# Optimization experiments

Measured on AMD Instinct MI355X. Metric: run time of the kernel, lower is better.

Reference implementation:

```python
import jax, jax.numpy as jnp
import numpy as np

B, N, D, R, W, H, I = 256, 2048, 128, 4, 1, 1024, 1024
CI = I + R * D                       # controller input size (1536)
IF = 2 * D * W + 2 * W + 1 + 4 * R + D * R   # interface size (787)
OPI = H + R * D                      # output_proj input (1536)


def _norm(v):
    # F.normalize(dim=-1): x / max(||x||, eps)
    return v / jnp.maximum(jnp.linalg.norm(v, axis=-1, keepdims=True), 1e-12)


def setup_inputs() -> dict:
    key = jax.random.key(0)
    ks = jax.random.split(key, 16)
    u = lambda k, shape, fan: jax.random.uniform(k, shape, jnp.float32, -1.0 / np.sqrt(fan), 1.0 / np.sqrt(fan))
    return {
        "x": jax.random.normal(ks[0], (B, I), jnp.float32),
        "memory": jax.random.normal(ks[1], (N, D), jnp.float32) * np.sqrt(2.0 / (N + D)),  # xavier-ish
        "usage": jax.random.uniform(ks[2], (N,), jnp.float32),          # usage in [0,1)
        "link": jax.random.normal(ks[3], (N, N), jnp.float32) * 0.01,   # non-trivial link state
        "W_ih": u(ks[4], (4 * H, CI), H),
        "W_hh": u(ks[5], (4 * H, H), H),
        "b_ih": u(ks[6], (4 * H,), H),
        "b_hh": u(ks[7], (4 * H,), H),
        "W_if": u(ks[8], (IF, H), H),
        "b_if": u(ks[9], (IF,), H),
        "W_out": u(ks[10], (H, OPI), OPI),
        "b_out": u(ks[11], (H,), OPI),
    }


def reference(x, memory, usage, link, W_ih, W_hh, b_ih, b_hh, W_if, b_if, W_out, b_out):
    # initial uniform read weights (prev state at first step)
    prev_rw = jnp.full((B, R, N), 1.0 / N, x.dtype)
    read_flat = (prev_rw @ memory).reshape(B, -1)                 # (B, R*D)
    cin = jnp.concatenate([x, read_flat], axis=-1)                # (B, CI)

    # single LSTM step, h0 = c0 = 0, torch gate order i,f,g,o
    g = cin @ W_ih.T + b_ih + b_hh
    gi, gf, gg, go = jnp.split(g, 4, axis=-1)
    c = jax.nn.sigmoid(gi) * jnp.tanh(gg)
    h = jax.nn.sigmoid(go) * jnp.tanh(c)                          # (B, H) controller out

    itf = h @ W_if.T + b_if                                       # (B, IF)
    o = 0
    write_vals = itf[:, o:o + D * W].reshape(B, W, D); o += D * W
    erase = jax.nn.sigmoid(itf[:, o:o + D * W]).reshape(B, W, D); o += D * W
    write_gates = jax.nn.sigmoid(itf[:, o:o + W]); o += W         # (B, W)
    alloc_gate = jax.nn.sigmoid(itf[:, o:o + 1]); o += 1          # (B, 1)
    o += W                                                        # free gates (parsed, unused)
    read_modes = jax.nn.softmax(itf[:, o:o + 3 * R].reshape(B, R, 3), -1); o += 3 * R
    read_str = jax.nn.softplus(itf[:, o:o + R]); o += R           # (B, R)
    read_keys = itf[:, o:o + D * R].reshape(B, R, D)

    # content addressing for the write (strength = 1)
    mem_n = _norm(memory)
    cw = jax.nn.softmax(_norm(write_vals.mean(1)) @ mem_n.T, -1)  # (B, N)

    # allocation weighting: sorted-usage cumprod (per source semantics)
    idx = jnp.argsort(usage)
    su = usage[idx]
    cp = jnp.cumprod(1.0 - su)
    alloc_s = jnp.concatenate([su[:1], su[1:] * cp[:-1]])
    alloc = jnp.zeros_like(usage).at[idx].set(alloc_s)[None, :] * alloc_gate  # (B, N)

    write_w = write_gates[:, :, None] * (0.5 * cw + 0.5 * alloc)[:, None, :]  # (B, W, N)

    # temporal link update: batch-mean of diag-masked outer product, decay 0.9
    lu = jnp.einsum('bwn,bwm->nm', write_w, write_w) / B
    lu = lu * (1.0 - jnp.eye(N, dtype=lu.dtype))
    link_new = link * 0.9 + lu * 0.1

    # memory write (erase then add, batch-mean)
    ev = erase * write_gates[:, :, None]
    av = write_vals * write_gates[:, :, None]
    erase_mat = jnp.einsum('bwn,bwd->nd', write_w, ev) / B
    add_mat = jnp.einsum('bwn,bwd->nd', write_w, av) / B
    mem_new = memory * (1.0 - erase_mat) + add_mat

    # read addressing on updated memory and updated link (all R heads vectorized)
    sim = jnp.einsum('brd,nd->brn', _norm(read_keys), _norm(mem_new))
    content_r = jax.nn.softmax(sim * read_str[:, :, None], -1)    # (B, R, N)
    backward_w = jnp.einsum('brn,nm->brm', prev_rw, link_new)     # mode 1: prev @ L
    forward_w = jnp.einsum('brn,mn->brm', prev_rw, link_new)      # mode 2: prev @ L^T
    new_rw = (read_modes[..., 0:1] * content_r
              + read_modes[..., 1:2] * backward_w
              + read_modes[..., 2:3] * forward_w)                 # (B, R, N)

    read_out = (new_rw @ mem_new).reshape(B, -1)                  # (B, R*D)
    out = jnp.concatenate([h, read_out], axis=-1) @ W_out.T + b_out
    return out
```

## Files before the change

kernel.cpp:

```cpp
#include <hip/hip_runtime.h>
#include <cmath>

#define DEVI __device__ __forceinline__

DEVI float sigm(float x){ return 1.f/(1.f+expf(-x)); }

typedef __attribute__((ext_vector_type(8))) _Float16 half8;
typedef __attribute__((ext_vector_type(4))) _Float16 half4;
typedef __attribute__((ext_vector_type(4))) float float4v;


__global__ void k_zero(float* __restrict__ p, int n){
  int i = blockIdx.x*256 + threadIdx.x;
  if (i < n) p[i] = 0.f;
}

__global__ __launch_bounds__(256) void k_stage1(
    const float* __restrict__ mem, float* __restrict__ cm, _Float16* __restrict__ mem_h,
    const float* __restrict__ usage, float* __restrict__ alloc,
    const float* __restrict__ link, float* __restrict__ rsl, float* __restrict__ csl)
{
  __shared__ float smem[4][132];
  const int blk = blockIdx.x, t = threadIdx.x;
  const int wv = t >> 6, lane = t & 63;

  if (blk < 32){
    int n0 = blk*64;
    float c0 = 0.f, c1 = 0.f;
    for (int r = wv; r < 64; r += 4){
      const float* a = mem + (size_t)(n0+r)*128;
      float x0 = a[lane], x1 = a[lane+64];
      float ss = x0*x0 + x1*x1;
      #pragma unroll
      for (int o = 1; o < 64; o <<= 1) ss += __shfl_xor(ss, o);
      float invn = 1.f / fmaxf(sqrtf(ss), 1e-12f);
      mem_h[(size_t)(n0+r)*128 + lane]      = (_Float16)(x0*invn);
      mem_h[(size_t)(n0+r)*128 + 64 + lane] = (_Float16)(x1*invn);
      c0 += x0; c1 += x1;
    }
    smem[wv][lane] = c0; smem[wv][64+lane] = c1;
    __syncthreads();
    if (t < 128) atomicAdd(&cm[t], smem[0][t]+smem[1][t]+smem[2][t]+smem[3][t]);
  } else if (blk < 160){
    int r0 = (blk - 32)*16;
    int c0 = t*8;
    float colacc[8];
    #pragma unroll
    for (int j = 0; j < 8; j++) colacc[j] = 0.f;
    for (int rg = 0; rg < 16; rg += 4){
      float4v v0[4], v1[4];
      #pragma unroll
      for (int u = 0; u < 4; u++){
        const float* lp = link + (size_t)(r0+rg+u)*2048 + c0;
        v0[u] = *(const float4v*)lp;
        v1[u] = *(const float4v*)(lp+4);
      }
      #pragma unroll
      for (int u = 0; u < 4; u++){
        float s = 0.f;
        #pragma unroll
        for (int j = 0; j < 4; j++){
          colacc[j]   += v0[u][j]; colacc[4+j] += v1[u][j];
          s += v0[u][j] + v1[u][j];
        }
        #pragma unroll
        for (int o = 32; o > 0; o >>= 1) s += __shfl_xor(s, o);
        if (lane == 0) smem[wv][rg+u] = s;
      }
    }
    __syncthreads();
    if (t < 16) rsl[r0+t] = smem[0][t]+smem[1][t]+smem[2][t]+smem[3][t];
    #pragma unroll
    for (int j = 0; j < 8; j++) atomicAdd(&csl[c0+j], colacc[j]);
  } else {
    int n = (blk - 160)*4 + wv;
    float un = usage[n];
    float prod = 1.f;
    #pragma unroll
    for (int i = 0; i < 32; i++){
      int m = lane + i*64;
      float um = usage[m];
      bool before = (um < un) || (um == un && m < n);
      prod *= before ? (1.f - um) : 1.f;
    }
    #pragma unroll
    for (int o = 32; o > 0; o >>= 1) prod *= __shfl_xor(prod, o);
    if (lane == 0) alloc[n] = un * prod;
  }
}

__global__ void k_cin(const float* __restrict__ x, const float* __restrict__ cm, _Float16* __restrict__ cin){
  int idx = blockIdx.x*256 + threadIdx.x;
  int b = idx / 1536, k = idx - b*1536;
  float v = (k < 1024) ? x[b*1024 + k] : cm[(k-1024) & 127] * (1.f/2048.f);
  cin[idx] = (_Float16)v;
}

__global__ void k_lstm(const float* __restrict__ g, _Float16* __restrict__ h){
  int idx = blockIdx.x*256 + threadIdx.x;
  int b = idx >> 10, j = idx & 1023;
  const float* gr = g + (size_t)b*4096;
  float c = sigm(gr[j]) * tanhf(gr[2048 + j]);
  h[idx] = (_Float16)(sigm(gr[3072 + j]) * tanhf(c));
}

#define QA 264
#define QB 520

template<typename TB> struct BReg;
template<> struct BReg<_Float16>{
  half8 v;
  DEVI void load(const _Float16* p){ v = *(const half8*)p; }
  DEVI half8 get() const { return v; }
};
template<> struct BReg<float>{
  float4v a, b;
  DEVI void load(const float* p){ a = *(const float4v*)p; b = *(const float4v*)(p+4); }
  DEVI half8 get() const {
    half8 h;
    #pragma unroll
    for (int j = 0; j < 4; j++){ h[j] = (_Float16)a[j]; h[4+j] = (_Float16)b[j]; }
    return h;
  }
};

template<typename TB>
__global__ __launch_bounds__(256) void gemm_t(
    const _Float16* __restrict__ A, const TB* __restrict__ Bm, float* __restrict__ C,
    int M, int N, int K,
    const float* __restrict__ bias1, const float* __restrict__ bias2)
{
  __shared__ _Float16 Ah[2][8*QA];
  __shared__ _Float16 Bh[2][8*QB];
  const int tid = threadIdx.x;
  const int m0 = blockIdx.y*32, n0 = blockIdx.x*64;
  const int T = K >> 6;
  const int arow = tid >> 3, aq = tid & 7;
  const int brow = tid >> 3, bq = tid & 7;
  int nB0 = n0 + brow;      if (nB0 >= N) nB0 = N - 1;
  int nB1 = n0 + brow + 32; if (nB1 >= N) nB1 = N - 1;
  const _Float16* Aptr = A + (size_t)(m0 + arow)*K + aq*8;
  const TB* Bp0 = Bm + (size_t)nB0*K + bq*8;
  const TB* Bp1 = Bm + (size_t)nB1*K + bq*8;
  const int wA  = aq*QA + arow*8;
  const int wB0 = bq*QB + brow*8;
  const int wB1 = bq*QB + (brow+32)*8;
  const int wv_ = tid >> 6, lane = tid & 63;
  const int fq = lane >> 4, fr = lane & 15;
  const int m16 = (wv_ & 1)*16, nb = (wv_ >> 1)*32;

  half8 ra;
  BReg<TB> rb0, rb1;
  ra = *(const half8*)(Aptr);
  rb0.load(Bp0);
  rb1.load(Bp1);
  *(half8*)&Ah[0][wA]  = ra;
  *(half8*)&Bh[0][wB0] = rb0.get();
  *(half8*)&Bh[0][wB1] = rb1.get();
  __syncthreads();

  float4v acc0 = {0.f,0.f,0.f,0.f}, acc1 = {0.f,0.f,0.f,0.f};
  for (int t = 0; t < T; t++){
    const int cur = t & 1, nxt = cur ^ 1;
    if (t+1 < T){
      ra = *(const half8*)(Aptr + (t+1)*64);
      rb0.load(Bp0 + (t+1)*64);
      rb1.load(Bp1 + (t+1)*64);
    }
    #pragma unroll
    for (int s = 0; s < 2; s++){
      int q = s*4 + fq;
      half8 a  = *(half8*)&Ah[cur][q*QA + (m16+fr)*8];
      half8 b0 = *(half8*)&Bh[cur][q*QB + (nb+fr)*8];
      half8 b1 = *(half8*)&Bh[cur][q*QB + (nb+16+fr)*8];
      acc0 = __builtin_amdgcn_mfma_f32_16x16x32_f16(a, b0, acc0, 0, 0, 0);
      acc1 = __builtin_amdgcn_mfma_f32_16x16x32_f16(a, b1, acc1, 0, 0, 0);
    }
    if (t+1 < T){
      *(half8*)&Ah[nxt][wA]  = ra;
      *(half8*)&Bh[nxt][wB0] = rb0.get();
      *(half8*)&Bh[nxt][wB1] = rb1.get();
    }
    __syncthreads();
  }

  const int colA = n0 + nb + fr, colB = colA + 16;
  #pragma unroll
  for (int i = 0; i < 4; i++){
    int m = m0 + m16 + fq*4 + i;
    if (colA < N){
      float v = acc0[i];
      if (bias1) v += bias1[colA];
      if (bias2) v += bias2[colA];
      C[(size_t)m*N + colA] = v;
    }
    if (colB < N){
      float v = acc1[i];
      if (bias1) v += bias1[colB];
      if (bias2) v += bias2[colB];
      C[(size_t)m*N + colB] = v;
    }
  }
}

DEVI float blockReduce128(float v, float* lds2){
  #pragma unroll
  for (int o = 32; o > 0; o >>= 1) v += __shfl_xor(v, o);
  int w = threadIdx.x >> 6;
  __syncthreads();
  if ((threadIdx.x & 63) == 0) lds2[w] = v;
  __syncthreads();
  return lds2[0] + lds2[1];
}

__global__ __launch_bounds__(128) void k_parse(const float* __restrict__ itf,
    _Float16* __restrict__ wv_h, float* __restrict__ ev, float* __restrict__ av,
    float* __restrict__ wg_, float* __restrict__ ag_,
    float* __restrict__ rm0, float* __restrict__ rm1, float* __restrict__ rm2,
    _Float16* __restrict__ rks_h)
{
  __shared__ float red[2];
  int b = blockIdx.x, t = threadIdx.x;
  const float* it = itf + (size_t)b*787;
  float wg = sigm(it[256]);
  float ag = sigm(it[257]);
  if (t == 0){ wg_[b] = wg; ag_[b] = ag; }
  float w = it[t];
  av[b*128 + t] = w * wg;
  ev[b*128 + t] = sigm(it[128 + t]) * wg;
  float ss = blockReduce128(w*w, red);
  float invwv = 1.f / fmaxf(sqrtf(ss), 1e-12f);
  wv_h[b*128 + t] = (_Float16)(w * invwv);
  if (t < 4){
    int rr = t;
    float m0v = it[259 + rr*3 + 0], m1v = it[259 + rr*3 + 1], m2v = it[259 + rr*3 + 2];
    float mx = fmaxf(m0v, fmaxf(m1v, m2v));
    float e0 = expf(m0v - mx), e1 = expf(m1v - mx), e2 = expf(m2v - mx);
    float inv = 1.f / (e0 + e1 + e2);
    rm0[b*4 + rr] = e0*inv; rm1[b*4 + rr] = e1*inv; rm2[b*4 + rr] = e2*inv;
  }
  #pragma unroll
  for (int rr = 0; rr < 4; rr++){
    float kv = it[275 + rr*128 + t];
    float ks = blockReduce128(kv*kv, red);
    float sx = it[271 + rr];
    float str = fmaxf(sx, 0.f) + log1pf(expf(-fabsf(sx)));
    float invk = 1.f / fmaxf(sqrtf(ks), 1e-12f);
    rks_h[((size_t)b*4 + rr)*128 + t] = (_Float16)(kv * invk * str);
  }
}

__global__ __launch_bounds__(256) void k_softmax_ww(float* __restrict__ P,
    const float* __restrict__ alloc, const float* __restrict__ wg, const float* __restrict__ ag){
  __shared__ float red[4];
  float* p = P + (size_t)blockIdx.x*2048;
  int t = threadIdx.x;
  float r[8];
  float mx = -3.4e38f;
  #pragma unroll
  for (int i = 0; i < 8; i++){ r[i] = p[t + i*256]; mx = fmaxf(mx, r[i]); }
  #pragma unroll
  for (int o = 32; o > 0; o >>= 1) mx = fmaxf(mx, __shfl_xor(mx, o));
  if ((t & 63) == 0) red[t >> 6] = mx;
  __syncthreads();
  mx = fmaxf(fmaxf(red[0], red[1]), fmaxf(red[2], red[3]));
  float s = 0.f;
  #pragma unroll
  for (int i = 0; i < 8; i++){ r[i] = expf(r[i] - mx); s += r[i]; }
  #pragma unroll
  for (int o = 32; o > 0; o >>= 1) s += __shfl_xor(s, o);
  __syncthreads();
  if ((t & 63) == 0) red[t >> 6] = s;
  __syncthreads();
  s = red[0] + red[1] + red[2] + red[3];
  float inv = 1.f / s;
  float wgb = wg[blockIdx.x], agb = ag[blockIdx.x];
  #pragma unroll
  for (int i = 0; i < 8; i++){
    int col = t + i*256;
    p[col] = wgb*(0.5f*r[i]*inv + 0.5f*alloc[col]*agb);
  }
}

__global__ __launch_bounds__(256) void k_bwfw(const float* __restrict__ ww,
                       const float* __restrict__ wg, const float* __restrict__ ag,
                       const float* __restrict__ alloc,
                       const float* __restrict__ rowsum, const float* __restrict__ colsum,
                       float* __restrict__ bw, float* __restrict__ fw){
  __shared__ float sq[4][64], sd[4][64];
  __shared__ float sred[4];
  __shared__ float tbs[256];
  int t = threadIdx.x & 63, z = threadIdx.x >> 6;
  int m = blockIdx.x*64 + t;
  float sa = 0.f;
  #pragma unroll
  for (int i = 0; i < 8; i++) sa += alloc[threadIdx.x + i*256];
  #pragma unroll
  for (int o = 32; o > 0; o >>= 1) sa += __shfl_xor(sa, o);
  if (t == 0) sred[z] = sa;
  __syncthreads();
  sa = (sred[0]+sred[1]) + (sred[2]+sred[3]);
  tbs[threadIdx.x] = wg[threadIdx.x]*(0.5f + 0.5f*ag[threadIdx.x]*sa);
  __syncthreads();
  float q = 0.f, dd = 0.f;
  for (int b = z*64; b < z*64 + 64; b += 4){
    float w0 = ww[(size_t)(b+0)*2048 + m];
    float w1 = ww[(size_t)(b+1)*2048 + m];
    float w2 = ww[(size_t)(b+2)*2048 + m];
    float w3 = ww[(size_t)(b+3)*2048 + m];
    q  = fmaf(tbs[b+0], w0, q);  dd = fmaf(w0, w0, dd);
    q  = fmaf(tbs[b+1], w1, q);  dd = fmaf(w1, w1, dd);
    q  = fmaf(tbs[b+2], w2, q);  dd = fmaf(w2, w2, dd);
    q  = fmaf(tbs[b+3], w3, q);  dd = fmaf(w3, w3, dd);
  }
  sq[z][t] = q; sd[z][t] = dd;
  __syncthreads();
  if (z == 0){
    q  = sq[0][t] + sq[1][t] + sq[2][t] + sq[3][t];
    dd = sd[0][t] + sd[1][t] + sd[2][t] + sd[3][t];
    float lus = (q - dd) * (1.f/256.f);
    bw[m] = (0.9f*colsum[m] + 0.1f*lus) * (1.f/2048.f);
    fw[m] = (0.9f*rowsum[m] + 0.1f*lus) * (1.f/2048.f);
  }
}

__global__ __launch_bounds__(256) void k_memupdate_fused(const float* __restrict__ ww,
    const float* __restrict__ ev, const float* __restrict__ av,
    const float* __restrict__ mem, const float* __restrict__ bw, const float* __restrict__ fw,
    _Float16* __restrict__ memn_h, _Float16* __restrict__ memnT_h,
    float* __restrict__ bwm, float* __restrict__ fwm)
{
  __shared__ float Ws[16][34];
  __shared__ float Es[16][132], Vs[16][132];
  __shared__ float lb[128], lf[128];
  __shared__ _Float16 Traw[32][132];
  const int n0 = blockIdx.x*32;
  const int tid = threadIdx.x, tx = tid & 31, ty = tid >> 5;
  if (tid < 128){ lb[tid] = 0.f; lf[tid] = 0.f; }
  const int wk = tid >> 4, wn = (tid & 15)*2;
  const int ek = tid >> 4, ec = (tid & 15)*8;
  float ae[4][4] = {}, aa[4][4] = {};
  for (int k0 = 0; k0 < 256; k0 += 16){
    float2 vw  = *(const float2*)(ww + (size_t)(k0+wk)*2048 + n0 + wn);
    float4 ve0 = *(const float4*)(ev + (size_t)(k0+ek)*128 + ec);
    float4 ve1 = *(const float4*)(ev + (size_t)(k0+ek)*128 + ec + 4);
    float4 va0 = *(const float4*)(av + (size_t)(k0+ek)*128 + ec);
    float4 va1 = *(const float4*)(av + (size_t)(k0+ek)*128 + ec + 4);
    __syncthreads();
    Ws[wk][wn] = vw.x; Ws[wk][wn+1] = vw.y;
    *(float4*)&Es[ek][ec] = ve0; *(float4*)&Es[ek][ec+4] = ve1;
    *(float4*)&Vs[ek][ec] = va0; *(float4*)&Vs[ek][ec+4] = va1;
    __syncthreads();
    #pragma unroll
    for (int k = 0; k < 16; k++){
      float a[4], e[4], v[4];
      #pragma unroll
      for (int i = 0; i < 4; i++) a[i] = Ws[k][ty*4+i];
      #pragma unroll
      for (int j = 0; j < 4; j++){ e[j] = Es[k][tx*4+j]; v[j] = Vs[k][tx*4+j]; }
      #pragma unroll
      for (int i = 0; i < 4; i++)
        #pragma unroll
        for (int j = 0; j < 4; j++){
          ae[i][j] = fmaf(a[i], e[j], ae[i][j]);
          aa[i][j] = fmaf(a[i], v[j], aa[i][j]);
        }
    }
  }
  float ab[4] = {0,0,0,0}, af[4] = {0,0,0,0};
  #pragma unroll
  for (int i = 0; i < 4; i++){
    int n = n0 + ty*4 + i;
    float bwn = bw[n], fwn = fw[n];
    float v[4]; float ss = 0.f;
    #pragma unroll
    for (int j = 0; j < 4; j++){
      int d = tx*4 + j;
      float em = ae[i][j]*(1.f/256.f), am = aa[i][j]*(1.f/256.f);
      float mv = mem[(size_t)n*128 + d]*(1.f - em) + am;
      v[j] = mv; ss += mv*mv;
      ab[j] = fmaf(bwn, mv, ab[j]);
      af[j] = fmaf(fwn, mv, af[j]);
    }
    #pragma unroll
    for (int o = 1; o < 32; o <<= 1) ss += __shfl_xor(ss, o);
    float invn = 1.f / fmaxf(sqrtf(ss), 1e-12f);
    half4 hn, hr;
    #pragma unroll
    for (int j = 0; j < 4; j++){ hn[j] = (_Float16)(v[j]*invn); hr[j] = (_Float16)v[j]; }
    *(half4*)(memn_h + (size_t)n*128 + tx*4) = hn;
    *(half4*)&Traw[ty*4+i][tx*4] = hr;
  }
  __syncthreads();
  {
    int d = tid >> 1, seg = (tid & 1)*16;
    half8 o0, o1;
    #pragma unroll
    for (int j = 0; j < 8; j++){ o0[j] = Traw[seg+j][d]; o1[j] = Traw[seg+8+j][d]; }
    *(half8*)(memnT_h + (size_t)d*2048 + n0 + seg)     = o0;
    *(half8*)(memnT_h + (size_t)d*2048 + n0 + seg + 8) = o1;
  }
  #pragma unroll
  for (int j = 0; j < 4; j++){
    atomicAdd(&lb[tx*4+j], ab[j]);
    atomicAdd(&lf[tx*4+j], af[j]);
  }
  __syncthreads();
  if (tid < 128){
    atomicAdd(&bwm[tid], lb[tid]);
    atomicAdd(&fwm[tid], lf[tid]);
  }
}

__global__ __launch_bounds__(256) void k_flash(
    const _Float16* __restrict__ Q, const _Float16* __restrict__ Kh,
    const _Float16* __restrict__ Vt,
    float* __restrict__ pacc, float* __restrict__ pm, float* __restrict__ pl)
{
  __shared__ _Float16 Pl[4][16][32];
  __shared__ float cmb[4][2080];
  __shared__ float scl[4][16];
  const int tid = threadIdx.x;
  const int qt = blockIdx.x >> 2, kc = blockIdx.x & 3;
  const int wv = tid >> 6, lane = tid & 63;
  const int fq = lane >> 4, fr = lane & 15;
  const int kw0 = kc*512 + wv*128;

  half8 aq[4];
  #pragma unroll
  for (int c = 0; c < 4; c++)
    aq[c] = *(const half8*)(Q + (size_t)(qt*16 + fr)*128 + c*32 + fq*8);

  float m[4] = {-3.0e38f,-3.0e38f,-3.0e38f,-3.0e38f};
  float l[4] = {0.f,0.f,0.f,0.f};
  float4v acc[8] = {};
  for (int s = 0; s < 4; s++){
    const int kb = kw0 + s*32;
    float4v S0 = {0,0,0,0}, S1 = {0,0,0,0};
    #pragma unroll
    for (int c = 0; c < 4; c++){
      half8 b0 = *(const half8*)(Kh + (size_t)(kb + fr)*128      + c*32 + fq*8);
      half8 b1 = *(const half8*)(Kh + (size_t)(kb + 16 + fr)*128 + c*32 + fq*8);
      S0 = __builtin_amdgcn_mfma_f32_16x16x32_f16(aq[c], b0, S0, 0, 0, 0);
      S1 = __builtin_amdgcn_mfma_f32_16x16x32_f16(aq[c], b1, S1, 0, 0, 0);
    }
    float mt[4], ps[4];
    #pragma unroll
    for (int i = 0; i < 4; i++) mt[i] = fmaxf(S0[i], S1[i]);
    #pragma unroll
    for (int o = 1; o < 16; o <<= 1){
      #pragma unroll
      for (int i = 0; i < 4; i++) mt[i] = fmaxf(mt[i], __shfl_xor(mt[i], o));
    }
    #pragma unroll
    for (int i = 0; i < 4; i++){
      float mn = fmaxf(m[i], mt[i]);
      float al = expf(m[i] - mn);
      float p0 = expf(S0[i] - mn), p1 = expf(S1[i] - mn);
      S0[i] = p0; S1[i] = p1;
      ps[i] = p0 + p1;
      l[i] *= al;
      m[i] = mn;
      #pragma unroll
      for (int c = 0; c < 8; c++) acc[c][i] *= al;
    }
    #pragma unroll
    for (int o = 1; o < 16; o <<= 1){
      #pragma unroll
      for (int i = 0; i < 4; i++) ps[i] += __shfl_xor(ps[i], o);
    }
    #pragma unroll
    for (int i = 0; i < 4; i++) l[i] += ps[i];
    #pragma unroll
    for (int i = 0; i < 4; i++){
      Pl[wv][fq*4+i][fr]      = (_Float16)S0[i];
      Pl[wv][fq*4+i][16 + fr] = (_Float16)S1[i];
    }
    half8 pf = *(half8*)&Pl[wv][fr][fq*8];
    #pragma unroll
    for (int c = 0; c < 8; c++){
      half8 bv = *(const half8*)(Vt + (size_t)(c*16 + fr)*2048 + kb + fq*8);
      acc[c] = __builtin_amdgcn_mfma_f32_16x16x32_f16(pf, bv, acc[c], 0, 0, 0);
    }
  }
  if (fr == 0){
    #pragma unroll
    for (int i = 0; i < 4; i++){
      cmb[wv][fq*4+i]      = m[i];
      cmb[wv][16 + fq*4+i] = l[i];
    }
  }
  #pragma unroll
  for (int c = 0; c < 8; c++)
    #pragma unroll
    for (int i = 0; i < 4; i++)
      cmb[wv][32 + (fq*4+i)*128 + c*16 + fr] = acc[c][i];
  __syncthreads();
  if (tid < 16){
    float mm = fmaxf(fmaxf(cmb[0][tid], cmb[1][tid]), fmaxf(cmb[2][tid], cmb[3][tid]));
    float ll = 0.f;
    #pragma unroll
    for (int w = 0; w < 4; w++){
      float e = expf(cmb[w][tid] - mm);
      scl[w][tid] = e;
      ll += e * cmb[w][16 + tid];
    }
    pm[blockIdx.x*16 + tid] = mm;
    pl[blockIdx.x*16 + tid] = ll;
  }
  __syncthreads();
  for (int e = tid; e < 2048; e += 256){
    int q = e >> 7;
    float a = scl[0][q]*cmb[0][32+e] + scl[1][q]*cmb[1][32+e]
            + scl[2][q]*cmb[2][32+e] + scl[3][q]*cmb[3][32+e];
    pacc[(size_t)blockIdx.x*2048 + e] = a;
  }
}

__global__ void k_hro_comb(const _Float16* __restrict__ h, const float* __restrict__ pacc,
                           const float* __restrict__ pm, const float* __restrict__ pl,
                           const float* __restrict__ rm0, const float* __restrict__ rm1,
                           const float* __restrict__ rm2, const float* __restrict__ bwm,
                           const float* __restrict__ fwm, _Float16* __restrict__ hro){
  int idx = blockIdx.x*256 + threadIdx.x;
  int b = idx / 1536, k = idx - b*1536;
  if (k < 1024){
    hro[idx] = h[b*1024 + k];
  } else {
    int r = k - 1024, rh = r >> 7, d = r & 127;
    int row = b*4 + rh, qt = row >> 4, q = row & 15;
    float mm = -3.0e38f;
    #pragma unroll
    for (int kc = 0; kc < 4; kc++) mm = fmaxf(mm, pm[(qt*4+kc)*16 + q]);
    float num = 0.f, den = 0.f;
    #pragma unroll
    for (int kc = 0; kc < 4; kc++){
      float e = expf(pm[(qt*4+kc)*16 + q] - mm);
      den += e * pl[(qt*4+kc)*16 + q];
      num += e * pacc[(size_t)(qt*4+kc)*2048 + q*128 + d];
    }
    float pv = num / den;
    hro[idx] = (_Float16)(rm0[row]*pv + rm1[row]*bwm[d] + rm2[row]*fwm[d]);
  }
}


extern "C" void kernel_launch(void* const* d_in, const int* in_sizes, int n_in,
                              void* d_out, int out_size, void* d_ws, size_t ws_size,
                              hipStream_t stream)
{
  const float* x     = (const float*)d_in[0];
  const float* mem   = (const float*)d_in[1];
  const float* usage = (const float*)d_in[2];
  const float* link  = (const float*)d_in[3];
  const float* W_ih  = (const float*)d_in[4];
  const float* b_ih  = (const float*)d_in[6];
  const float* b_hh  = (const float*)d_in[7];
  const float* W_if  = (const float*)d_in[8];
  const float* b_if  = (const float*)d_in[9];
  const float* W_out = (const float*)d_in[10];
  const float* b_out = (const float*)d_in[11];
  float* out = (float*)d_out;
  float* ws  = (float*)d_ws;

  float* cm     = ws + 0;
  float* csl    = ws + 128;
  float* bwm    = ws + 2176;
  float* fwm    = ws + 2304;
  float* bw     = ws + 2688;
  float* fw     = ws + 4736;
  float* wg     = ws + 6784;
  float* ag     = ws + 7040;
  float* rm0    = ws + 7296;
  float* rm1    = ws + 8320;
  float* rm2    = ws + 9344;
  float* alloc  = ws + 10368;
  float* rsl    = ws + 12416;
  float* ev     = ws + 14464;
  float* av     = ws + 47232;
  float* g      = ws + 80000;
  float* itf    = ws + 1128576;
  float* ww     = ws + 1330048;
  float* pacc   = ws + 1854336;
  float* pm     = ws + 2378624;
  float* pl     = ws + 2382720;
  _Float16* wv_h    = (_Float16*)(ws + 2386816);
  _Float16* mem_h   = (_Float16*)(ws + 2403200);
  _Float16* memn_h  = (_Float16*)(ws + 2534272);
  _Float16* memnT_h = (_Float16*)(ws + 2665344);
  _Float16* rks_h   = (_Float16*)(ws + 2796416);
  _Float16* hro_h   = (_Float16*)(ws + 2861952);
  _Float16* cin_h   = (_Float16*)(ws + 3058560);
  _Float16* h_h     = (_Float16*)(ws + 3255168);

  k_zero<<<10, 256, 0, stream>>>(ws, 2432);

  k_stage1<<<672, 256, 0, stream>>>(mem, cm, mem_h, usage, alloc, link, rsl, csl);
  k_cin   <<<1536, 256, 0, stream>>>(x, cm, cin_h);

  gemm_t<float><<<dim3(64,8), 256, 0, stream>>>(cin_h, W_ih, g, 256, 4096, 1536, b_ih, b_hh);
  k_lstm<<<1024, 256, 0, stream>>>(g, h_h);

  gemm_t<float><<<dim3(13,8), 256, 0, stream>>>(h_h, W_if, itf, 256, 787, 1024, b_if, nullptr);
  k_parse<<<256, 128, 0, stream>>>(itf, wv_h, ev, av, wg, ag, rm0, rm1, rm2, rks_h);

  gemm_t<_Float16><<<dim3(32,8), 256, 0, stream>>>(wv_h, mem_h, ww, 256, 2048, 128, nullptr, nullptr);
  k_softmax_ww<<<256, 256, 0, stream>>>(ww, alloc, wg, ag);

  k_bwfw<<<32, 256, 0, stream>>>(ww, wg, ag, alloc, rsl, csl, bw, fw);

  k_memupdate_fused<<<64, 256, 0, stream>>>(ww, ev, av, mem, bw, fw, memn_h, memnT_h, bwm, fwm);

  k_flash<<<256, 256, 0, stream>>>(rks_h, memn_h, memnT_h, pacc, pm, pl);

  k_hro_comb<<<1536, 256, 0, stream>>>(h_h, pacc, pm, pl, rm0, rm1, rm2, bwm, fwm, hro_h);
  gemm_t<float><<<dim3(16,8), 256, 0, stream>>>(hro_h, W_out, out, 256, 1024, 1536, b_out, nullptr);

  (void)in_sizes; (void)n_in; (void)out_size; (void)ws_size;
}
```

Measured before the change: 269.2 us.

## Widen stage1 parallelism and replace column-sum atomics with two-pass partial reduction

```diff
diff --git a/kernel.cpp b/kernel.cpp
--- a/kernel.cpp
+++ b/kernel.cpp
@@ -18,62 +18,81 @@
 __global__ __launch_bounds__(256) void k_stage1(
     const float* __restrict__ mem, float* __restrict__ cm, _Float16* __restrict__ mem_h,
     const float* __restrict__ usage, float* __restrict__ alloc,
-    const float* __restrict__ link, float* __restrict__ rsl, float* __restrict__ csl)
+    const float* __restrict__ link, float* __restrict__ rsl, float* __restrict__ cslp)
 {
   __shared__ float smem[4][132];
   const int blk = blockIdx.x, t = threadIdx.x;
   const int wv = t >> 6, lane = t & 63;
 
-  if (blk < 32){
-    int n0 = blk*64;
+  if (blk < 128){
+    int rbase = blk*16 + wv*4;
+    float x0[4], x1[4], ss[4];
+    #pragma unroll
+    for (int u = 0; u < 4; u++){
+      const float* a = mem + (size_t)(rbase+u)*128;
+      x0[u] = a[lane]; x1[u] = a[lane+64];
+    }
+    #pragma unroll
+    for (int u = 0; u < 4; u++) ss[u] = x0[u]*x0[u] + x1[u]*x1[u];
+    #pragma unroll
+    for (int o = 1; o < 64; o <<= 1){
+      #pragma unroll
+      for (int u = 0; u < 4; u++) ss[u] += __shfl_xor(ss[u], o);
+    }
     float c0 = 0.f, c1 = 0.f;
-    for (int r = wv; r < 64; r += 4){
-      const float* a = mem + (size_t)(n0+r)*128;
-      float x0 = a[lane], x1 = a[lane+64];
-      float ss = x0*x0 + x1*x1;
-      #pragma unroll
-      for (int o = 1; o < 64; o <<= 1) ss += __shfl_xor(ss, o);
-      float invn = 1.f / fmaxf(sqrtf(ss), 1e-12f);
-      mem_h[(size_t)(n0+r)*128 + lane]      = (_Float16)(x0*invn);
-      mem_h[(size_t)(n0+r)*128 + 64 + lane] = (_Float16)(x1*invn);
-      c0 += x0; c1 += x1;
+    #pragma unroll
+    for (int u = 0; u < 4; u++){
+      float invn = 1.f / fmaxf(sqrtf(ss[u]), 1e-12f);
+      mem_h[(size_t)(rbase+u)*128 + lane]      = (_Float16)(x0[u]*invn);
+      mem_h[(size_t)(rbase+u)*128 + 64 + lane] = (_Float16)(x1[u]*invn);
+      c0 += x0[u]; c1 += x1[u];
     }
     smem[wv][lane] = c0; smem[wv][64+lane] = c1;
     __syncthreads();
     if (t < 128) atomicAdd(&cm[t], smem[0][t]+smem[1][t]+smem[2][t]+smem[3][t]);
-  } else if (blk < 160){
-    int r0 = (blk - 32)*16;
+  } else if (blk < 384){
+    int pb = blk - 128;
+    int r0 = pb*8;
     int c0 = t*8;
+    float4v v0[8], v1[8];
+    #pragma unroll
+    for (int u = 0; u < 8; u++){
+      const float* lp = link + (size_t)(r0+u)*2048 + c0;
+      v0[u] = *(const float4v*)lp;
+      v1[u] = *(const float4v*)(lp+4);
+    }
     float colacc[8];
     #pragma unroll
     for (int j = 0; j < 8; j++) colacc[j] = 0.f;
-    for (int rg = 0; rg < 16; rg += 4){
-      float4v v0[4], v1[4];
-      #pragma unroll
-      for (int u = 0; u < 4; u++){
-        const float* lp = link + (size_t)(r0+rg+u)*2048 + c0;
-        v0[u] = *(const float4v*)lp;
-        v1[u] = *(const float4v*)(lp+4);
+    float rowpart[8];
+    #pragma unroll
+    for (int u = 0; u < 8; u++){
+      float s = 0.f;
+      #pragma unroll
+      for (int j = 0; j < 4; j++){
+        colacc[j]   += v0[u][j]; colacc[4+j] += v1[u][j];
+        s += v0[u][j] + v1[u][j];
       }
-      #pragma unroll
-      for (int u = 0; u < 4; u++){
-        float s = 0.f;
-        #pragma unroll
-        for (int j = 0; j < 4; j++){
-          colacc[j]   += v0[u][j]; colacc[4+j] += v1[u][j];
-          s += v0[u][j] + v1[u][j];
-        }
-        #pragma unroll
-        for (int o = 32; o > 0; o >>= 1) s += __shfl_xor(s, o);
-        if (lane == 0) smem[wv][rg+u] = s;
-      }
+      rowpart[u] = s;
+    }
+    #pragma unroll
+    for (int o = 1; o < 64; o <<= 1){
+      #pragma unroll
+      for (int u = 0; u < 8; u++) rowpart[u] += __shfl_xor(rowpart[u], o);
+    }
+    if (lane == 0){
+      #pragma unroll
+      for (int u = 0; u < 8; u++) smem[wv][u] = rowpart[u];
     }
     __syncthreads();
-    if (t < 16) rsl[r0+t] = smem[0][t]+smem[1][t]+smem[2][t]+smem[3][t];
-    #pragma unroll
-    for (int j = 0; j < 8; j++) atomicAdd(&csl[c0+j], colacc[j]);
+    if (t < 8) rsl[r0+t] = smem[0][t]+smem[1][t]+smem[2][t]+smem[3][t];
+    float4v w0, w1;
+    #pragma unroll
+    for (int j = 0; j < 4; j++){ w0[j] = colacc[j]; w1[j] = colacc[4+j]; }
+    *(float4v*)&cslp[(size_t)pb*2048 + c0]     = w0;
+    *(float4v*)&cslp[(size_t)pb*2048 + c0 + 4] = w1;
   } else {
-    int n = (blk - 160)*4 + wv;
+    int n = (blk - 384)*4 + wv;
     float un = usage[n];
     float prod = 1.f;
     #pragma unroll
@@ -89,11 +108,30 @@
   }
 }
 
-__global__ void k_cin(const float* __restrict__ x, const float* __restrict__ cm, _Float16* __restrict__ cin){
-  int idx = blockIdx.x*256 + threadIdx.x;
-  int b = idx / 1536, k = idx - b*1536;
-  float v = (k < 1024) ? x[b*1024 + k] : cm[(k-1024) & 127] * (1.f/2048.f);
-  cin[idx] = (_Float16)v;
+__global__ __launch_bounds__(256) void k_cin_csl(const float* __restrict__ x,
+    const float* __restrict__ cm, _Float16* __restrict__ cin,
+    const float* __restrict__ cslp, float* __restrict__ csl)
+{
+  __shared__ float sm[4][64];
+  int blk = blockIdx.x, t = threadIdx.x;
+  if (blk < 1536){
+    int idx = blk*256 + t;
+    int b = idx / 1536, k = idx - b*1536;
+    float v = (k < 1024) ? x[b*1024 + k] : cm[(k-1024) & 127] * (1.f/2048.f);
+    cin[idx] = (_Float16)v;
+  } else {
+    int j = blk - 1536;
+    int tl = t & 63, q = t >> 6;
+    int col = j*64 + tl;
+    float s = 0.f;
+    for (int p = q*64; p < q*64 + 64; p += 4){
+      s += cslp[(size_t)(p+0)*2048 + col] + cslp[(size_t)(p+1)*2048 + col]
+         + cslp[(size_t)(p+2)*2048 + col] + cslp[(size_t)(p+3)*2048 + col];
+    }
+    sm[q][tl] = s;
+    __syncthreads();
+    if (q == 0) csl[col] = sm[0][tl]+sm[1][tl]+sm[2][tl]+sm[3][tl];
+  }
 }
 
 __global__ void k_lstm(const float* __restrict__ g, _Float16* __restrict__ h){
@@ -592,11 +630,12 @@
   _Float16* hro_h   = (_Float16*)(ws + 2861952);
   _Float16* cin_h   = (_Float16*)(ws + 3058560);
   _Float16* h_h     = (_Float16*)(ws + 3255168);
+  float* cslp       = ws + 3386240;
 
   k_zero<<<10, 256, 0, stream>>>(ws, 2432);
 
-  k_stage1<<<672, 256, 0, stream>>>(mem, cm, mem_h, usage, alloc, link, rsl, csl);
-  k_cin   <<<1536, 256, 0, stream>>>(x, cm, cin_h);
+  k_stage1<<<896, 256, 0, stream>>>(mem, cm, mem_h, usage, alloc, link, rsl, cslp);
+  k_cin_csl<<<1568, 256, 0, stream>>>(x, cm, cin_h, cslp, csl);
 
   gemm_t<float><<<dim3(64,8), 256, 0, stream>>>(cin_h, W_ih, g, 256, 4096, 1536, b_ih, b_hh);
   k_lstm<<<1024, 256, 0, stream>>>(g, h_h);
```

Measured after the change: 236.3 us. -12.2%, faster.
